# Kernel tuning notes

Measured on AMD Instinct MI355X. Metric: run time of the kernel, lower is better.

The kernel has to match this reference:

```python
import jax, jax.numpy as jnp
import numpy as np

NTYPES = 2
NATOMS = (512, 512)
N = 1024          # total atoms
NN = 128          # neighbors per type
M = NTYPES * NN   # 256 neighbor slots per atom
D = 25            # last embedding width
FH = 240          # fitting hidden width
B = 8
RMIN, RMAX = 5.8, 6.0


def _embed_mlp(s, W0, b0, W1, b1, W2, b2):
    # DeepMD-style resnet embedding net: 1 -> D -> D -> D, tanh + skip
    h = jnp.tanh(s @ W0 + b0)
    h = h + jnp.tanh(h @ W1 + b1)
    h = h + jnp.tanh(h @ W2 + b2)
    return h


def setup_inputs() -> dict:
    key = jax.random.key(0)
    ks = jax.random.split(key, 20)
    # relative positions; components in [-4.5, 4.5] so |r| spans <5.8, [5.8,6.0), >=6.0
    image_dR = (jax.random.uniform(ks[0], (B, N, NTYPES, NN, 3), jnp.float32) - 0.5) * 9.0
    # 0 == empty neighbor slot (mask = list_neigh > 0); index-1 in [0, N)
    list_neigh = jax.random.randint(ks[1], (B, N, NTYPES, NN), 0, 1025)
    davg = 0.1 * jax.random.normal(ks[2], (NTYPES, M, 4), jnp.float32)
    dstd = jax.random.uniform(ks[3], (NTYPES, M, 4), jnp.float32, 0.5, 1.5)
    P = NTYPES * NTYPES
    eW0 = jax.random.normal(ks[4], (P, 1, D), jnp.float32)
    eb0 = 0.1 * jax.random.normal(ks[5], (P, D), jnp.float32)
    eW1 = jax.random.normal(ks[6], (P, D, D), jnp.float32) / np.sqrt(D)
    eb1 = 0.1 * jax.random.normal(ks[7], (P, D), jnp.float32)
    eW2 = jax.random.normal(ks[8], (P, D, D), jnp.float32) / np.sqrt(D)
    eb2 = 0.1 * jax.random.normal(ks[9], (P, D), jnp.float32)
    fW0 = jax.random.normal(ks[10], (NTYPES, 16 * D, FH), jnp.float32) / np.sqrt(16 * D)
    fb0 = 0.1 * jax.random.normal(ks[11], (NTYPES, FH), jnp.float32)
    fW1 = jax.random.normal(ks[12], (NTYPES, FH, FH), jnp.float32) / np.sqrt(FH)
    fb1 = 0.1 * jax.random.normal(ks[13], (NTYPES, FH), jnp.float32)
    fW2 = jax.random.normal(ks[14], (NTYPES, FH, FH), jnp.float32) / np.sqrt(FH)
    fb2 = 0.1 * jax.random.normal(ks[15], (NTYPES, FH), jnp.float32)
    fW3 = jax.random.normal(ks[16], (NTYPES, FH, 1), jnp.float32) / np.sqrt(FH)
    fb3 = 0.1 * jax.random.normal(ks[17], (NTYPES, 1), jnp.float32)
    ener_shift = 0.01 * jax.random.normal(ks[18], (NTYPES,), jnp.float32)
    return {
        'image_dR': image_dR, 'list_neigh': list_neigh,
        'davg': davg, 'dstd': dstd,
        'eW0': eW0, 'eb0': eb0, 'eW1': eW1, 'eb1': eb1, 'eW2': eW2, 'eb2': eb2,
        'fW0': fW0, 'fb0': fb0, 'fW1': fW1, 'fb1': fb1, 'fW2': fW2, 'fb2': fb2,
        'fW3': fW3, 'fb3': fb3, 'ener_shift': ener_shift,
        'dfeat': jnp.zeros((1,), jnp.float32),
        'Egroup_weight': jnp.zeros((1,), jnp.float32),
        'divider': jnp.ones((1,), jnp.float32),
    }


def _forward(image_dR, list_neigh, davg, dstd,
             eW0, eb0, eW1, eb1, eW2, eb2,
             fW0, fb0, fW1, fb1, fW2, fb2, fW3, fb3, ener_shift):
    dR = image_dR.reshape(B, N, M, 3)
    neigh = list_neigh.reshape(B, N, M)
    mask = neigh > 0
    mf = mask.astype(dR.dtype)
    dR2 = jnp.sum(dR * dR, axis=-1)                       # [B,N,M]
    safe_dR2 = jnp.where(mask, dR2, 1.0)
    Rij = jnp.sqrt(safe_dR2)
    inr = mf / Rij                                        # 1/|r|, 0 off-mask
    x = Rij * mf                                          # nr = dR2/Rij = |r|
    Ri_xyz = dR / safe_dR2[..., None] * mf[..., None]     # r / |r|^2
    inr2 = inr * inr
    inr4 = inr2 * inr2
    inr3 = inr4 * x
    # smooth switching function on [RMIN, RMAX]
    u = (x - RMIN) / (RMAX - RMIN)
    poly = u * u * u * (-6.0 * u * u + 15.0 * u - 10.0) + 1.0
    dpoly = (3.0 * u * u * (-6.0 * u * u + 15.0 * u - 10.0)
             + u * u * u * (-12.0 * u + 15.0)) / (RMAX - RMIN)
    mid = (x >= RMIN) & (x < RMAX)
    vv = jnp.where(x < RMIN, 1.0, jnp.where(mid, poly, 0.0)) * mf
    dvv = jnp.where(mid, dpoly, 0.0) * mf
    Ri_pre = jnp.concatenate([inr[..., None], Ri_xyz], axis=-1)   # [B,N,M,4]
    common = (dvv * inr)[..., None] * dR                          # [B,N,M,3]
    row0 = dR * (inr3 * vv)[..., None] - Ri_pre[..., 0:1] * common
    eye = jnp.eye(3, dtype=dR.dtype)
    outer = (2.0 * dR[..., :, None] * dR[..., None, :] * inr4[..., None, None]
             - eye * inr2[..., None, None])                       # [B,N,M,3,3]
    rows = outer * vv[..., None, None] - Ri_pre[..., 1:4, None] * common[..., None, :]
    Ri_d = jnp.concatenate([row0[..., None, :], rows], axis=-2) * mf[..., None, None]  # [B,N,M,4,3]
    Ri = Ri_pre * vv[..., None]
    # per-type normalization stats broadcast over atoms of each type
    davg_res = jnp.concatenate([jnp.broadcast_to(davg[t], (NATOMS[t], M, 4)) for t in range(NTYPES)], axis=0)
    dstd_res = jnp.concatenate([jnp.broadcast_to(dstd[t], (NATOMS[t], M, 4)) for t in range(NTYPES)], axis=0)
    Ri = (Ri - davg_res) / dstd_res
    Ri_d = Ri_d / dstd_res[..., None]

    def ei_fn(Ri_n):
        Ei_list = []
        start = 0
        for t in range(NTYPES):
            na = NATOMS[t]
            Rt = jax.lax.slice_in_dim(Ri_n, start, start + na, axis=1)  # [B,na,M,4]
            acc = jnp.zeros((B, na, 4, D), Ri_n.dtype)
            for t1 in range(NTYPES):
                p = t * NTYPES + t1
                blk = Rt[:, :, t1 * NN:(t1 + 1) * NN]                  # [B,na,NN,4]
                G = _embed_mlp(blk[..., 0:1], eW0[p], eb0[p], eW1[p], eb1[p], eW2[p], eb2[p])
                acc = acc + jnp.einsum('bnkd,bnke->bnde', blk, G)
            acc = acc * (4.0 / (NN * NTYPES * 4))
            DRt = jnp.einsum('bnde,bndf->bnef', acc, acc[..., :16]).reshape(B, na, D * 16)
            h = jnp.tanh(DRt @ fW0[t] + fb0[t])
            h = h + jnp.tanh(h @ fW1[t] + fb1[t])
            h = h + jnp.tanh(h @ fW2[t] + fb2[t])
            Ei_list.append(h @ fW3[t] + fb3[t] + ener_shift[t])
            start += na
        return jnp.concatenate(Ei_list, axis=1)   # [B,N,1]

    Ei, vjpf = jax.vjp(ei_fn, Ri)
    dE, = vjpf(jnp.ones_like(Ei))                 # dEi/dRi  [B,N,M,4]
    Etot = jnp.sum(Ei, axis=1)                    # [B,1]
    pair = jnp.einsum('bnmd,bnmdx->bnmx', dE, Ri_d)   # per-pair force term [B,N,M,3]
    F_self = -jnp.sum(pair, axis=2)
    j = neigh - 1
    valid = j >= 0
    flat_idx = jnp.where(valid, j, N) + jnp.arange(B)[:, None, None] * (N + 1)
    contrib = jnp.where(valid[..., None], pair, 0.0)
    seg = jax.ops.segment_sum(contrib.reshape(-1, 3), flat_idx.reshape(-1), num_segments=B * (N + 1))
    F = F_self + seg.reshape(B, N + 1, 3)[:, :N]
    return Etot, Ei, F


def reference(image_dR, list_neigh, davg, dstd,
              eW0, eb0, eW1, eb1, eW2, eb2,
              fW0, fb0, fW1, fb1, fW2, fb2, fW3, fb3, ener_shift,
              dfeat, Egroup_weight, divider):
    # dfeat / Egroup_weight / divider are in the torch forward signature but unused
    return _forward(image_dR, list_neigh, davg, dstd,
                    eW0, eb0, eW1, eb1, eW2, eb2,
                    fW0, fb0, fW1, fb1, fW2, fb2, fW3, fb3, ener_shift)
```

## Files before the change

### kernel.cpp

```cpp
#include <hip/hip_runtime.h>

#define DEV __device__ __forceinline__

namespace {

constexpr int B_ = 8;
constexpr int N_ = 1024;
constexpr int M_ = 256;
constexpr int D_ = 25;
constexpr int FH_ = 240;
constexpr int NATOM = B_ * N_;
constexpr float CSC = 1.0f / 256.0f;

DEV float fast_tanh(float x) {
  float ax = fabsf(x);
  float e = __expf(-2.0f * ax);
  float r = (1.0f - e) * __builtin_amdgcn_rcpf(1.0f + e);
  return copysignf(r, x);
}

struct Geom {
  float mf, inr, inr2, inr4, inr3, vv, dvv;
};

DEV Geom geom_core(float dx, float dy, float dz, int nb) {
  Geom g;
  g.mf = (nb > 0) ? 1.0f : 0.0f;
  float dr2 = dx * dx + dy * dy + dz * dz;
  float safe = (nb > 0) ? dr2 : 1.0f;
  float rs = __builtin_amdgcn_rsqf(safe);
  float rij = safe * rs;
  g.inr = g.mf * rs;
  float x = rij * g.mf;
  g.inr2 = g.inr * g.inr;
  g.inr4 = g.inr2 * g.inr2;
  g.inr3 = g.inr4 * x;
  float u = (x - 5.8f) * 5.0f;
  float uu = u * u;
  float A = -6.0f * uu + 15.0f * u - 10.0f;
  float poly = uu * u * A + 1.0f;
  float dpoly = (3.0f * uu * A + uu * u * (-12.0f * u + 15.0f)) * 5.0f;
  bool mid = (x >= 5.8f) && (x < 6.0f);
  g.vv = ((x < 5.8f) ? 1.0f : (mid ? poly : 0.0f)) * g.mf;
  g.dvv = (mid ? dpoly : 0.0f) * g.mf;
  return g;
}

DEV void geom_blk(const Geom& g, float dx, float dy, float dz, int t, int m,
                  const float* __restrict__ davg, const float* __restrict__ dstd,
                  float* __restrict__ blk, float* __restrict__ rsv) {
  int bidx = (t * M_ + m) * 4;
  float4 av = *(const float4*)(davg + bidx);
  float4 sv = *(const float4*)(dstd + bidx);
  float pre[4] = {g.inr, dx * g.inr2, dy * g.inr2, dz * g.inr2};
  float avf[4] = {av.x, av.y, av.z, av.w};
  float svf[4] = {sv.x, sv.y, sv.z, sv.w};
#pragma unroll
  for (int d = 0; d < 4; ++d) {
    rsv[d] = __builtin_amdgcn_rcpf(svf[d]);
    blk[d] = (pre[d] * g.vv - avf[d]) * rsv[d];
  }
}

__global__ __launch_bounds__(256) void k_embed_acc(
    const float* __restrict__ dR, const int* __restrict__ neigh,
    const float* __restrict__ davg, const float* __restrict__ dstd,
    const float* __restrict__ eW0, const float* __restrict__ eb0,
    const float* __restrict__ eW1, const float* __restrict__ eb1,
    const float* __restrict__ eW2, const float* __restrict__ eb2,
    float* __restrict__ acc_ws) {
  __shared__ float sG[M_ * D_];
  __shared__ float4 sBlk[M_];
  int atom = blockIdx.x;
  int n = atom & (N_ - 1);
  int t = (n >= 512) ? 1 : 0;
  int m = threadIdx.x;
  int p = __builtin_amdgcn_readfirstlane(t * 2 + (m >> 7));
  const float* W0 = eW0 + p * D_;
  const float* b0 = eb0 + p * D_;
  const float* W1 = eW1 + p * D_ * D_;
  const float* b1 = eb1 + p * D_;
  const float* W2 = eW2 + p * D_ * D_;
  const float* b2 = eb2 + p * D_;
  int base = atom * M_ + m;
  float dx = dR[base * 3 + 0];
  float dy = dR[base * 3 + 1];
  float dz = dR[base * 3 + 2];
  int nb = neigh[base];
  Geom g = geom_core(dx, dy, dz, nb);
  float blk[4], rsv[4];
  geom_blk(g, dx, dy, dz, t, m, davg, dstd, blk, rsv);
  float s = blk[0];
  float h[D_], a[D_];
#pragma unroll
  for (int e = 0; e < D_; ++e) h[e] = fast_tanh(fmaf(s, W0[e], b0[e]));
#pragma unroll
  for (int e = 0; e < D_; ++e) a[e] = b1[e];
#pragma unroll
  for (int f = 0; f < D_; ++f) {
    float hf = h[f];
#pragma unroll
    for (int e = 0; e < D_; ++e) a[e] = fmaf(hf, W1[f * D_ + e], a[e]);
  }
#pragma unroll
  for (int e = 0; e < D_; ++e) h[e] += fast_tanh(a[e]);
#pragma unroll
  for (int e = 0; e < D_; ++e) a[e] = b2[e];
#pragma unroll
  for (int f = 0; f < D_; ++f) {
    float hf = h[f];
#pragma unroll
    for (int e = 0; e < D_; ++e) a[e] = fmaf(hf, W2[f * D_ + e], a[e]);
  }
#pragma unroll
  for (int e = 0; e < D_; ++e) sG[m * D_ + e] = h[e] + fast_tanh(a[e]);
  sBlk[m] = make_float4(blk[0], blk[1], blk[2], blk[3]);
  __syncthreads();
  if (threadIdx.x < 100) {
    int d = threadIdx.x & 3;
    int e = threadIdx.x >> 2;
    const float* sb = (const float*)sBlk;
    float s0 = 0.0f, s1 = 0.0f, s2 = 0.0f, s3 = 0.0f;
    for (int mm = 0; mm < M_; mm += 4) {
      s0 = fmaf(sb[(mm + 0) * 4 + d], sG[(mm + 0) * D_ + e], s0);
      s1 = fmaf(sb[(mm + 1) * 4 + d], sG[(mm + 1) * D_ + e], s1);
      s2 = fmaf(sb[(mm + 2) * 4 + d], sG[(mm + 2) * D_ + e], s2);
      s3 = fmaf(sb[(mm + 3) * 4 + d], sG[(mm + 3) * D_ + e], s3);
    }
    acc_ws[atom * 100 + d * D_ + e] = ((s0 + s1) + (s2 + s3)) * CSC;
  }
}

__global__ __launch_bounds__(256) void k_fit(
    const float* __restrict__ acc_ws,
    const float* __restrict__ fW0, const float* __restrict__ fb0,
    const float* __restrict__ fW1, const float* __restrict__ fb1,
    const float* __restrict__ fW2, const float* __restrict__ fb2,
    const float* __restrict__ fW3, const float* __restrict__ fb3,
    const float* __restrict__ ener_shift,
    float* __restrict__ dacc_ws, float* __restrict__ out) {
  constexpr int AB = 8;
  __shared__ float sAcc[AB][100];
  __shared__ float sX[AB][400];
  __shared__ float sH0[AB][FH_];
  __shared__ float sT1[AB][FH_];
  __shared__ float sH1[AB][FH_];
  __shared__ float sT2[AB][FH_];
  __shared__ float sEi[AB];
  int a0 = blockIdx.x * AB;
  int bb = a0 >> 10;
  int n0 = a0 & (N_ - 1);
  int t = (n0 >= 512) ? 1 : 0;
  int tid = threadIdx.x;
  for (int idx = tid; idx < AB * 100; idx += 256)
    ((float*)sAcc)[idx] = acc_ws[a0 * 100 + idx];
  if (tid < AB) sEi[tid] = 0.0f;
  __syncthreads();
  for (int idx = tid; idx < AB * 400; idx += 256) {
    int a = idx / 400; int r = idx % 400; int e = r >> 4; int f = r & 15;
    const float* A = sAcc[a];
    sX[a][r] = A[e] * A[f] + A[25 + e] * A[25 + f] + A[50 + e] * A[50 + f] +
               A[75 + e] * A[75 + f];
  }
  __syncthreads();
  const float* W0 = fW0 + t * 400 * FH_;
  const float* W1 = fW1 + t * FH_ * FH_;
  const float* W2 = fW2 + t * FH_ * FH_;
  const float* B0 = fb0 + t * FH_;
  const float* B1 = fb1 + t * FH_;
  const float* B2 = fb2 + t * FH_;
  const float* W3 = fW3 + t * FH_;
  int j = tid;
  if (j < FH_) {
    float acc8[AB];
#pragma unroll
    for (int a = 0; a < AB; ++a) acc8[a] = B0[j];
    for (int i = 0; i < 400; ++i) {
      float w = W0[i * FH_ + j];
#pragma unroll
      for (int a = 0; a < AB; ++a) acc8[a] = fmaf(sX[a][i], w, acc8[a]);
    }
#pragma unroll
    for (int a = 0; a < AB; ++a) sH0[a][j] = fast_tanh(acc8[a]);
  }
  __syncthreads();
  if (j < FH_) {
    float acc8[AB];
#pragma unroll
    for (int a = 0; a < AB; ++a) acc8[a] = B1[j];
    for (int f = 0; f < FH_; ++f) {
      float w = W1[f * FH_ + j];
#pragma unroll
      for (int a = 0; a < AB; ++a) acc8[a] = fmaf(sH0[a][f], w, acc8[a]);
    }
#pragma unroll
    for (int a = 0; a < AB; ++a) {
      float tv = fast_tanh(acc8[a]);
      sT1[a][j] = tv;
      sH1[a][j] = sH0[a][j] + tv;
    }
  }
  __syncthreads();
  if (j < FH_) {
    float acc8[AB];
#pragma unroll
    for (int a = 0; a < AB; ++a) acc8[a] = B2[j];
    for (int f = 0; f < FH_; ++f) {
      float w = W2[f * FH_ + j];
#pragma unroll
      for (int a = 0; a < AB; ++a) acc8[a] = fmaf(sH1[a][f], w, acc8[a]);
    }
    float w3 = W3[j];
#pragma unroll
    for (int a = 0; a < AB; ++a) {
      float tv = fast_tanh(acc8[a]);
      sT2[a][j] = tv;
      atomicAdd(&sEi[a], (sH1[a][j] + tv) * w3);
    }
  }
  __syncthreads();
  if (tid < AB) {
    float ei = sEi[tid] + fb3[t] + ener_shift[t];
    out[8 + a0 + tid] = ei;
    atomicAdd(&out[bb], ei);
  }
  if (j < FH_) {
    float w3 = W3[j];
#pragma unroll
    for (int a = 0; a < AB; ++a) {
      float tv = sT2[a][j];
      sT2[a][j] = w3 * (1.0f - tv * tv);
    }
  }
  __syncthreads();
  if (j < FH_) {
    float w3 = W3[j];
    float acc8[AB];
#pragma unroll
    for (int a = 0; a < AB; ++a) acc8[a] = w3;
    for (int k = 0; k < FH_; ++k) {
      float w = W2[j * FH_ + k];
#pragma unroll
      for (int a = 0; a < AB; ++a) acc8[a] = fmaf(sT2[a][k], w, acc8[a]);
    }
#pragma unroll
    for (int a = 0; a < AB; ++a) {
      float dh1 = acc8[a];
      float tv = sT1[a][j];
      sH1[a][j] = dh1;
      sT1[a][j] = dh1 * (1.0f - tv * tv);
    }
  }
  __syncthreads();
  if (j < FH_) {
    float acc8[AB];
#pragma unroll
    for (int a = 0; a < AB; ++a) acc8[a] = sH1[a][j];
    for (int k = 0; k < FH_; ++k) {
      float w = W1[j * FH_ + k];
#pragma unroll
      for (int a = 0; a < AB; ++a) acc8[a] = fmaf(sT1[a][k], w, acc8[a]);
    }
#pragma unroll
    for (int a = 0; a < AB; ++a) {
      float h0v = sH0[a][j];
      sH0[a][j] = acc8[a] * (1.0f - h0v * h0v);
    }
  }
  __syncthreads();
  for (int i = tid; i < 400; i += 256) {
    float acc8[AB];
#pragma unroll
    for (int a = 0; a < AB; ++a) acc8[a] = 0.0f;
    for (int jj = 0; jj < FH_; ++jj) {
      float w = W0[i * FH_ + jj];
#pragma unroll
      for (int a = 0; a < AB; ++a) acc8[a] = fmaf(sH0[a][jj], w, acc8[a]);
    }
#pragma unroll
    for (int a = 0; a < AB; ++a) sX[a][i] = acc8[a];
  }
  __syncthreads();
  for (int idx = tid; idx < AB * 100; idx += 256) {
    int a = idx / 100; int r = idx % 100; int d = r / 25; int e = r % 25;
    const float* A = sAcc[a];
    const float* DX = sX[a];
    float sum = 0.0f;
#pragma unroll
    for (int f = 0; f < 16; ++f) sum = fmaf(DX[e * 16 + f], A[d * 25 + f], sum);
    if (e < 16) {
#pragma unroll
      for (int e2 = 0; e2 < 25; ++e2) sum = fmaf(DX[e2 * 16 + e], A[d * 25 + e2], sum);
    }
    dacc_ws[a0 * 100 + idx] = sum;
  }
}

__global__ __launch_bounds__(256) __attribute__((amdgpu_waves_per_eu(2, 5)))
void k_bwd_force(
    const float* __restrict__ dR, const int* __restrict__ neigh,
    const float* __restrict__ davg, const float* __restrict__ dstd,
    const float* __restrict__ eW0, const float* __restrict__ eb0,
    const float* __restrict__ eW1, const float* __restrict__ eb1,
    const float* __restrict__ eW2, const float* __restrict__ eb2,
    const float* __restrict__ dacc_ws, float* __restrict__ out) {
  int atom = blockIdx.x;
  int bb = atom >> 10;
  int n = atom & (N_ - 1);
  int t = (n >= 512) ? 1 : 0;
  int m = threadIdx.x;
  int p = __builtin_amdgcn_readfirstlane(t * 2 + (m >> 7));
  const float* W0 = eW0 + p * D_;
  const float* b0 = eb0 + p * D_;
  const float* W1 = eW1 + p * D_ * D_;
  const float* b1 = eb1 + p * D_;
  const float* W2 = eW2 + p * D_ * D_;
  const float* b2 = eb2 + p * D_;
  const float* dac = dacc_ws + atom * 100;
  int base = atom * M_ + m;
  float dx = dR[base * 3 + 0];
  float dy = dR[base * 3 + 1];
  float dz = dR[base * 3 + 2];
  int nb = neigh[base];
  Geom g = geom_core(dx, dy, dz, nb);
  float blk[4], rsv[4];
  geom_blk(g, dx, dy, dz, t, m, davg, dstd, blk, rsv);

  float s = blk[0];
  float h[D_], hp[D_];
#pragma unroll
  for (int e = 0; e < D_; ++e) {
    float th = fast_tanh(fmaf(s, W0[e], b0[e]));
    h[e] = th;
    hp[e] = (1.0f - th * th) * W0[e];
  }
  {
    float a[D_], ap[D_];
#pragma unroll
    for (int e = 0; e < D_; ++e) { a[e] = b1[e]; ap[e] = 0.0f; }
#pragma unroll
    for (int f = 0; f < D_; ++f) {
      float hf = h[f], gf = hp[f];
#pragma unroll
      for (int e = 0; e < D_; ++e) {
        float w = W1[f * D_ + e];
        a[e] = fmaf(hf, w, a[e]);
        ap[e] = fmaf(gf, w, ap[e]);
      }
    }
#pragma unroll
    for (int e = 0; e < D_; ++e) {
      float th = fast_tanh(a[e]);
      h[e] += th;
      hp[e] = fmaf(1.0f - th * th, ap[e], hp[e]);
    }
  }
  {
    float a[D_], ap[D_];
#pragma unroll
    for (int e = 0; e < D_; ++e) { a[e] = b2[e]; ap[e] = 0.0f; }
#pragma unroll
    for (int f = 0; f < D_; ++f) {
      float hf = h[f], gf = hp[f];
#pragma unroll
      for (int e = 0; e < D_; ++e) {
        float w = W2[f * D_ + e];
        a[e] = fmaf(hf, w, a[e]);
        ap[e] = fmaf(gf, w, ap[e]);
      }
    }
#pragma unroll
    for (int e = 0; e < D_; ++e) {
      float th = fast_tanh(a[e]);
      h[e] += th;
      hp[e] = fmaf(1.0f - th * th, ap[e], hp[e]);
    }
  }

  float ds = 0.0f, db0 = 0.0f, db1 = 0.0f, db2 = 0.0f, db3 = 0.0f;
#pragma unroll
  for (int e = 0; e < D_; ++e) {
    float d0 = dac[e], d1 = dac[25 + e], d2 = dac[50 + e], d3 = dac[75 + e];
    float gG = d0 * blk[0] + d1 * blk[1] + d2 * blk[2] + d3 * blk[3];
    ds = fmaf(gG, hp[e], ds);
    float he = h[e];
    db0 = fmaf(d0, he, db0);
    db1 = fmaf(d1, he, db1);
    db2 = fmaf(d2, he, db2);
    db3 = fmaf(d3, he, db3);
  }
  float dE0 = (db0 + ds) * CSC;
  float dE1 = db1 * CSC, dE2 = db2 * CSC, dE3 = db3 * CSC;

  float dv[3] = {dx, dy, dz};
  float pre1[3] = {dx * g.inr2, dy * g.inr2, dz * g.inr2};
  float ci = g.dvv * g.inr;
  float com[3];
#pragma unroll
  for (int c = 0; c < 3; ++c) com[c] = ci * dv[c];
  float iv = g.inr3 * g.vv;
  float pc[3];
  float f0 = dE0 * rsv[0];
#pragma unroll
  for (int c = 0; c < 3; ++c) pc[c] = f0 * (dv[c] * iv - g.inr * com[c]);
  float dEr[3] = {dE1, dE2, dE3};
#pragma unroll
  for (int r = 0; r < 3; ++r) {
    float fr = dEr[r] * rsv[1 + r];
#pragma unroll
    for (int c = 0; c < 3; ++c) {
      float outer = 2.0f * dv[r] * dv[c] * g.inr4 - ((r == c) ? g.inr2 : 0.0f);
      pc[c] = fmaf(fr, outer * g.vv - pre1[r] * com[c], pc[c]);
    }
  }
  float px = pc[0] * g.mf, py = pc[1] * g.mf, pz = pc[2] * g.mf;

  if (nb > 0) {
    int jn = nb - 1;
    int fi = 8 + NATOM + (bb * N_ + jn) * 3;
    atomicAdd(&out[fi + 0], px);
    atomicAdd(&out[fi + 1], py);
    atomicAdd(&out[fi + 2], pz);
  }
#pragma unroll
  for (int i = 1; i < 64; i <<= 1) {
    px += __shfl_xor(px, i);
    py += __shfl_xor(py, i);
    pz += __shfl_xor(pz, i);
  }
  if ((m & 63) == 0) {
    int fi = 8 + NATOM + atom * 3;
    atomicAdd(&out[fi + 0], -px);
    atomicAdd(&out[fi + 1], -py);
    atomicAdd(&out[fi + 2], -pz);
  }
}

}

extern "C" void kernel_launch(void* const* d_in, const int* in_sizes, int n_in,
                              void* d_out, int out_size, void* d_ws, size_t ws_size,
                              hipStream_t stream) {
  (void)in_sizes; (void)n_in; (void)ws_size;
  const float* image_dR   = (const float*)d_in[0];
  const int*   list_neigh = (const int*)d_in[1];
  const float* davg       = (const float*)d_in[2];
  const float* dstd       = (const float*)d_in[3];
  const float* eW0        = (const float*)d_in[4];
  const float* eb0        = (const float*)d_in[5];
  const float* eW1        = (const float*)d_in[6];
  const float* eb1        = (const float*)d_in[7];
  const float* eW2        = (const float*)d_in[8];
  const float* eb2        = (const float*)d_in[9];
  const float* fW0        = (const float*)d_in[10];
  const float* fb0        = (const float*)d_in[11];
  const float* fW1        = (const float*)d_in[12];
  const float* fb1        = (const float*)d_in[13];
  const float* fW2        = (const float*)d_in[14];
  const float* fb2        = (const float*)d_in[15];
  const float* fW3        = (const float*)d_in[16];
  const float* fb3        = (const float*)d_in[17];
  const float* ener_shift = (const float*)d_in[18];
  float* out = (float*)d_out;
  float* acc_ws  = (float*)d_ws;
  float* dacc_ws = acc_ws + NATOM * 100;

  hipMemsetAsync(d_out, 0, (size_t)out_size * sizeof(float), stream);
  k_embed_acc<<<NATOM, 256, 0, stream>>>(image_dR, list_neigh, davg, dstd,
                                         eW0, eb0, eW1, eb1, eW2, eb2, acc_ws);
  k_fit<<<NATOM / 8, 256, 0, stream>>>(acc_ws, fW0, fb0, fW1, fb1, fW2, fb2,
                                       fW3, fb3, ener_shift, dacc_ws, out);
  k_bwd_force<<<NATOM, 256, 0, stream>>>(image_dR, list_neigh, davg, dstd,
                                         eW0, eb0, eW1, eb1, eW2, eb2,
                                         dacc_ws, out);
}
```

Before: 948.4 us.

## Interleave fitting activations for float4 LDS reads and stage embed weights in LDS

The fitting kernel's shared activation buffers change from [atom][feature] to [feature][atom] layout, so each inner-loop step reads all 8 atoms with two float4 LDS loads instead of eight scalar loads. The backward-force kernel now copies the embedding weights (padded to 28-wide rows) and the per-atom dacc vector into shared memory once per block, and reads them with vectorized LDS loads instead of per-thread global/scalar loads. Its waves-per-EU upper bound is also raised. The weight staging adds a syncthreads and some LDS traffic per block, and the larger register arrays may raise register pressure.

New measurement: 944.0 us. Within noise of the previous version (-0.5%).

```diff
diff --git a/kernel.cpp b/kernel.cpp
--- a/kernel.cpp
+++ b/kernel.cpp
@@ -11,6 +11,8 @@
 constexpr int FH_ = 240;
 constexpr int NATOM = B_ * N_;
 constexpr float CSC = 1.0f / 256.0f;
+constexpr int WROW = 28;
+constexpr int WPAIR = 4 * WROW + 2 * D_ * WROW;
 
 DEV float fast_tanh(float x) {
   float ax = fabsf(x);
@@ -59,6 +61,42 @@
   for (int d = 0; d < 4; ++d) {
     rsv[d] = __builtin_amdgcn_rcpf(svf[d]);
     blk[d] = (pre[d] * g.vv - avf[d]) * rsv[d];
+  }
+}
+
+DEV void load_wrow(const float* __restrict__ wr, float* __restrict__ wrow) {
+#pragma unroll
+  for (int k = 0; k < 7; ++k) {
+    float4 qv = ((const float4*)wr)[k];
+    wrow[4 * k + 0] = qv.x;
+    wrow[4 * k + 1] = qv.y;
+    wrow[4 * k + 2] = qv.z;
+    wrow[4 * k + 3] = qv.w;
+  }
+}
+
+DEV void stage_weights(int tid, int t,
+                       const float* __restrict__ eW0, const float* __restrict__ eb0,
+                       const float* __restrict__ eW1, const float* __restrict__ eb1,
+                       const float* __restrict__ eW2, const float* __restrict__ eb2,
+                       float* __restrict__ sW) {
+  for (int idx = tid; idx < 2 * WPAIR; idx += 256) {
+    int pl = idx / WPAIR;
+    int r = idx - pl * WPAIR;
+    int pp = t * 2 + pl;
+    float v = 0.0f;
+    if (r < 28) { if (r < 25) v = eW0[pp * 25 + r]; }
+    else if (r < 56) { int e = r - 28; if (e < 25) v = eb0[pp * 25 + e]; }
+    else if (r < 84) { int e = r - 56; if (e < 25) v = eb1[pp * 25 + e]; }
+    else if (r < 112) { int e = r - 84; if (e < 25) v = eb2[pp * 25 + e]; }
+    else if (r < 112 + D_ * WROW) {
+      int rr = r - 112; int f = rr / WROW, e = rr - f * WROW;
+      if (e < 25) v = eW1[pp * 625 + f * 25 + e];
+    } else {
+      int rr = r - (112 + D_ * WROW); int f = rr / WROW, e = rr - f * WROW;
+      if (e < 25) v = eW2[pp * 625 + f * 25 + e];
+    }
+    sW[idx] = v;
   }
 }
 
@@ -141,11 +179,11 @@
     float* __restrict__ dacc_ws, float* __restrict__ out) {
   constexpr int AB = 8;
   __shared__ float sAcc[AB][100];
-  __shared__ float sX[AB][400];
-  __shared__ float sH0[AB][FH_];
-  __shared__ float sT1[AB][FH_];
-  __shared__ float sH1[AB][FH_];
-  __shared__ float sT2[AB][FH_];
+  __shared__ __align__(16) float sX[400 * AB];
+  __shared__ __align__(16) float sH0[FH_ * AB];
+  __shared__ __align__(16) float sT1[FH_ * AB];
+  __shared__ __align__(16) float sH1[FH_ * AB];
+  __shared__ __align__(16) float sT2[FH_ * AB];
   __shared__ float sEi[AB];
   int a0 = blockIdx.x * AB;
   int bb = a0 >> 10;
@@ -159,8 +197,8 @@
   for (int idx = tid; idx < AB * 400; idx += 256) {
     int a = idx / 400; int r = idx % 400; int e = r >> 4; int f = r & 15;
     const float* A = sAcc[a];
-    sX[a][r] = A[e] * A[f] + A[25 + e] * A[25 + f] + A[50 + e] * A[50 + f] +
-               A[75 + e] * A[75 + f];
+    sX[r * AB + a] = A[e] * A[f] + A[25 + e] * A[25 + f] +
+                     A[50 + e] * A[50 + f] + A[75 + e] * A[75 + f];
   }
   __syncthreads();
   const float* W0 = fW0 + t * 400 * FH_;
@@ -177,11 +215,18 @@
     for (int a = 0; a < AB; ++a) acc8[a] = B0[j];
     for (int i = 0; i < 400; ++i) {
       float w = W0[i * FH_ + j];
-#pragma unroll
-      for (int a = 0; a < AB; ++a) acc8[a] = fmaf(sX[a][i], w, acc8[a]);
-    }
-#pragma unroll
-    for (int a = 0; a < AB; ++a) sH0[a][j] = fast_tanh(acc8[a]);
+      const float4* xr = (const float4*)(sX + i * AB);
+      float4 x0 = xr[0], x1 = xr[1];
+      acc8[0] = fmaf(x0.x, w, acc8[0]); acc8[1] = fmaf(x0.y, w, acc8[1]);
+      acc8[2] = fmaf(x0.z, w, acc8[2]); acc8[3] = fmaf(x0.w, w, acc8[3]);
+      acc8[4] = fmaf(x1.x, w, acc8[4]); acc8[5] = fmaf(x1.y, w, acc8[5]);
+      acc8[6] = fmaf(x1.z, w, acc8[6]); acc8[7] = fmaf(x1.w, w, acc8[7]);
+    }
+    float4* h0 = (float4*)(sH0 + j * AB);
+    h0[0] = make_float4(fast_tanh(acc8[0]), fast_tanh(acc8[1]),
+                        fast_tanh(acc8[2]), fast_tanh(acc8[3]));
+    h0[1] = make_float4(fast_tanh(acc8[4]), fast_tanh(acc8[5]),
+                        fast_tanh(acc8[6]), fast_tanh(acc8[7]));
   }
   __syncthreads();
   if (j < FH_) {
@@ -190,14 +235,18 @@
     for (int a = 0; a < AB; ++a) acc8[a] = B1[j];
     for (int f = 0; f < FH_; ++f) {
       float w = W1[f * FH_ + j];
-#pragma unroll
-      for (int a = 0; a < AB; ++a) acc8[a] = fmaf(sH0[a][f], w, acc8[a]);
+      const float4* hr = (const float4*)(sH0 + f * AB);
+      float4 h0a = hr[0], h0b = hr[1];
+      acc8[0] = fmaf(h0a.x, w, acc8[0]); acc8[1] = fmaf(h0a.y, w, acc8[1]);
+      acc8[2] = fmaf(h0a.z, w, acc8[2]); acc8[3] = fmaf(h0a.w, w, acc8[3]);
+      acc8[4] = fmaf(h0b.x, w, acc8[4]); acc8[5] = fmaf(h0b.y, w, acc8[5]);
+      acc8[6] = fmaf(h0b.z, w, acc8[6]); acc8[7] = fmaf(h0b.w, w, acc8[7]);
     }
 #pragma unroll
     for (int a = 0; a < AB; ++a) {
       float tv = fast_tanh(acc8[a]);
-      sT1[a][j] = tv;
-      sH1[a][j] = sH0[a][j] + tv;
+      sT1[j * AB + a] = tv;
+      sH1[j * AB + a] = sH0[j * AB + a] + tv;
     }
   }
   __syncthreads();
@@ -207,15 +256,19 @@
     for (int a = 0; a < AB; ++a) acc8[a] = B2[j];
     for (int f = 0; f < FH_; ++f) {
       float w = W2[f * FH_ + j];
-#pragma unroll
-      for (int a = 0; a < AB; ++a) acc8[a] = fmaf(sH1[a][f], w, acc8[a]);
+      const float4* hr = (const float4*)(sH1 + f * AB);
+      float4 h1a = hr[0], h1b = hr[1];
+      acc8[0] = fmaf(h1a.x, w, acc8[0]); acc8[1] = fmaf(h1a.y, w, acc8[1]);
+      acc8[2] = fmaf(h1a.z, w, acc8[2]); acc8[3] = fmaf(h1a.w, w, acc8[3]);
+      acc8[4] = fmaf(h1b.x, w, acc8[4]); acc8[5] = fmaf(h1b.y, w, acc8[5]);
+      acc8[6] = fmaf(h1b.z, w, acc8[6]); acc8[7] = fmaf(h1b.w, w, acc8[7]);
     }
     float w3 = W3[j];
 #pragma unroll
     for (int a = 0; a < AB; ++a) {
       float tv = fast_tanh(acc8[a]);
-      sT2[a][j] = tv;
-      atomicAdd(&sEi[a], (sH1[a][j] + tv) * w3);
+      sT2[j * AB + a] = tv;
+      atomicAdd(&sEi[a], (sH1[j * AB + a] + tv) * w3);
     }
   }
   __syncthreads();
@@ -228,8 +281,8 @@
     float w3 = W3[j];
 #pragma unroll
     for (int a = 0; a < AB; ++a) {
-      float tv = sT2[a][j];
-      sT2[a][j] = w3 * (1.0f - tv * tv);
+      float tv = sT2[j * AB + a];
+      sT2[j * AB + a] = w3 * (1.0f - tv * tv);
     }
   }
   __syncthreads();
@@ -240,31 +293,39 @@
     for (int a = 0; a < AB; ++a) acc8[a] = w3;
     for (int k = 0; k < FH_; ++k) {
       float w = W2[j * FH_ + k];
-#pragma unroll
-      for (int a = 0; a < AB; ++a) acc8[a] = fmaf(sT2[a][k], w, acc8[a]);
+      const float4* gr = (const float4*)(sT2 + k * AB);
+      float4 g2a = gr[0], g2b = gr[1];
+      acc8[0] = fmaf(g2a.x, w, acc8[0]); acc8[1] = fmaf(g2a.y, w, acc8[1]);
+      acc8[2] = fmaf(g2a.z, w, acc8[2]); acc8[3] = fmaf(g2a.w, w, acc8[3]);
+      acc8[4] = fmaf(g2b.x, w, acc8[4]); acc8[5] = fmaf(g2b.y, w, acc8[5]);
+      acc8[6] = fmaf(g2b.z, w, acc8[6]); acc8[7] = fmaf(g2b.w, w, acc8[7]);
     }
 #pragma unroll
     for (int a = 0; a < AB; ++a) {
       float dh1 = acc8[a];
-      float tv = sT1[a][j];
-      sH1[a][j] = dh1;
-      sT1[a][j] = dh1 * (1.0f - tv * tv);
+      float tv = sT1[j * AB + a];
+      sH1[j * AB + a] = dh1;
+      sT1[j * AB + a] = dh1 * (1.0f - tv * tv);
     }
   }
   __syncthreads();
   if (j < FH_) {
     float acc8[AB];
 #pragma unroll
-    for (int a = 0; a < AB; ++a) acc8[a] = sH1[a][j];
+    for (int a = 0; a < AB; ++a) acc8[a] = sH1[j * AB + a];
     for (int k = 0; k < FH_; ++k) {
       float w = W1[j * FH_ + k];
-#pragma unroll
-      for (int a = 0; a < AB; ++a) acc8[a] = fmaf(sT1[a][k], w, acc8[a]);
+      const float4* gr = (const float4*)(sT1 + k * AB);
+      float4 g1a = gr[0], g1b = gr[1];
+      acc8[0] = fmaf(g1a.x, w, acc8[0]); acc8[1] = fmaf(g1a.y, w, acc8[1]);
+      acc8[2] = fmaf(g1a.z, w, acc8[2]); acc8[3] = fmaf(g1a.w, w, acc8[3]);
+      acc8[4] = fmaf(g1b.x, w, acc8[4]); acc8[5] = fmaf(g1b.y, w, acc8[5]);
+      acc8[6] = fmaf(g1b.z, w, acc8[6]); acc8[7] = fmaf(g1b.w, w, acc8[7]);
     }
 #pragma unroll
     for (int a = 0; a < AB; ++a) {
-      float h0v = sH0[a][j];
-      sH0[a][j] = acc8[a] * (1.0f - h0v * h0v);
+      float h0v = sH0[j * AB + a];
+      sH0[j * AB + a] = acc8[a] * (1.0f - h0v * h0v);
     }
   }
   __syncthreads();
@@ -274,29 +335,35 @@
     for (int a = 0; a < AB; ++a) acc8[a] = 0.0f;
     for (int jj = 0; jj < FH_; ++jj) {
       float w = W0[i * FH_ + jj];
-#pragma unroll
-      for (int a = 0; a < AB; ++a) acc8[a] = fmaf(sH0[a][jj], w, acc8[a]);
-    }
-#pragma unroll
-    for (int a = 0; a < AB; ++a) sX[a][i] = acc8[a];
+      const float4* gr = (const float4*)(sH0 + jj * AB);
+      float4 g0a = gr[0], g0b = gr[1];
+      acc8[0] = fmaf(g0a.x, w, acc8[0]); acc8[1] = fmaf(g0a.y, w, acc8[1]);
+      acc8[2] = fmaf(g0a.z, w, acc8[2]); acc8[3] = fmaf(g0a.w, w, acc8[3]);
+      acc8[4] = fmaf(g0b.x, w, acc8[4]); acc8[5] = fmaf(g0b.y, w, acc8[5]);
+      acc8[6] = fmaf(g0b.z, w, acc8[6]); acc8[7] = fmaf(g0b.w, w, acc8[7]);
+    }
+    float4* xw = (float4*)(sX + i * AB);
+    xw[0] = make_float4(acc8[0], acc8[1], acc8[2], acc8[3]);
+    xw[1] = make_float4(acc8[4], acc8[5], acc8[6], acc8[7]);
   }
   __syncthreads();
   for (int idx = tid; idx < AB * 100; idx += 256) {
     int a = idx / 100; int r = idx % 100; int d = r / 25; int e = r % 25;
     const float* A = sAcc[a];
-    const float* DX = sX[a];
     float sum = 0.0f;
 #pragma unroll
-    for (int f = 0; f < 16; ++f) sum = fmaf(DX[e * 16 + f], A[d * 25 + f], sum);
+    for (int f = 0; f < 16; ++f)
+      sum = fmaf(sX[(e * 16 + f) * AB + a], A[d * 25 + f], sum);
     if (e < 16) {
 #pragma unroll
-      for (int e2 = 0; e2 < 25; ++e2) sum = fmaf(DX[e2 * 16 + e], A[d * 25 + e2], sum);
+      for (int e2 = 0; e2 < 25; ++e2)
+        sum = fmaf(sX[(e2 * 16 + e) * AB + a], A[d * 25 + e2], sum);
     }
     dacc_ws[a0 * 100 + idx] = sum;
   }
 }
 
-__global__ __launch_bounds__(256) __attribute__((amdgpu_waves_per_eu(2, 5)))
+__global__ __launch_bounds__(256) __attribute__((amdgpu_waves_per_eu(2, 8)))
 void k_bwd_force(
     const float* __restrict__ dR, const int* __restrict__ neigh,
     const float* __restrict__ davg, const float* __restrict__ dstd,
@@ -304,19 +371,17 @@
     const float* __restrict__ eW1, const float* __restrict__ eb1,
     const float* __restrict__ eW2, const float* __restrict__ eb2,
     const float* __restrict__ dacc_ws, float* __restrict__ out) {
+  __shared__ __align__(16) float sW[2 * WPAIR];
+  __shared__ float sDac[100];
   int atom = blockIdx.x;
   int bb = atom >> 10;
   int n = atom & (N_ - 1);
   int t = (n >= 512) ? 1 : 0;
   int m = threadIdx.x;
-  int p = __builtin_amdgcn_readfirstlane(t * 2 + (m >> 7));
-  const float* W0 = eW0 + p * D_;
-  const float* b0 = eb0 + p * D_;
-  const float* W1 = eW1 + p * D_ * D_;
-  const float* b1 = eb1 + p * D_;
-  const float* W2 = eW2 + p * D_ * D_;
-  const float* b2 = eb2 + p * D_;
-  const float* dac = dacc_ws + atom * 100;
+  stage_weights(m, t, eW0, eb0, eW1, eb1, eW2, eb2, sW);
+  for (int idx = m; idx < 100; idx += 256) sDac[idx] = dacc_ws[atom * 100 + idx];
+  __syncthreads();
+  const float* wp = sW + (m >> 7) * WPAIR;
   int base = atom * M_ + m;
   float dx = dR[base * 3 + 0];
   float dy = dR[base * 3 + 1];
@@ -328,24 +393,34 @@
 
   float s = blk[0];
   float h[D_], hp[D_];
-#pragma unroll
-  for (int e = 0; e < D_; ++e) {
-    float th = fast_tanh(fmaf(s, W0[e], b0[e]));
-    h[e] = th;
-    hp[e] = (1.0f - th * th) * W0[e];
+  {
+    float w0r[WROW], b0r[WROW];
+    load_wrow(wp, w0r);
+    load_wrow(wp + WROW, b0r);
+#pragma unroll
+    for (int e = 0; e < D_; ++e) {
+      float th = fast_tanh(fmaf(s, w0r[e], b0r[e]));
+      h[e] = th;
+      hp[e] = (1.0f - th * th) * w0r[e];
+    }
   }
   {
     float a[D_], ap[D_];
-#pragma unroll
-    for (int e = 0; e < D_; ++e) { a[e] = b1[e]; ap[e] = 0.0f; }
+    {
+      float b1r[WROW];
+      load_wrow(wp + 2 * WROW, b1r);
+#pragma unroll
+      for (int e = 0; e < D_; ++e) { a[e] = b1r[e]; ap[e] = 0.0f; }
+    }
 #pragma unroll
     for (int f = 0; f < D_; ++f) {
+      float wrow[WROW];
+      load_wrow(wp + 4 * WROW + f * WROW, wrow);
       float hf = h[f], gf = hp[f];
 #pragma unroll
       for (int e = 0; e < D_; ++e) {
-        float w = W1[f * D_ + e];
-        a[e] = fmaf(hf, w, a[e]);
-        ap[e] = fmaf(gf, w, ap[e]);
+        a[e] = fmaf(hf, wrow[e], a[e]);
+        ap[e] = fmaf(gf, wrow[e], ap[e]);
       }
     }
 #pragma unroll
@@ -357,16 +432,21 @@
   }
   {
     float a[D_], ap[D_];
-#pragma unroll
-    for (int e = 0; e < D_; ++e) { a[e] = b2[e]; ap[e] = 0.0f; }
+    {
+      float b2r[WROW];
+      load_wrow(wp + 3 * WROW, b2r);
+#pragma unroll
+      for (int e = 0; e < D_; ++e) { a[e] = b2r[e]; ap[e] = 0.0f; }
+    }
 #pragma unroll
     for (int f = 0; f < D_; ++f) {
+      float wrow[WROW];
+      load_wrow(wp + (4 + D_) * WROW + f * WROW, wrow);
       float hf = h[f], gf = hp[f];
 #pragma unroll
       for (int e = 0; e < D_; ++e) {
-        float w = W2[f * D_ + e];
-        a[e] = fmaf(hf, w, a[e]);
-        ap[e] = fmaf(gf, w, ap[e]);
+        a[e] = fmaf(hf, wrow[e], a[e]);
+        ap[e] = fmaf(gf, wrow[e], ap[e]);
       }
     }
 #pragma unroll
@@ -380,7 +460,7 @@
   float ds = 0.0f, db0 = 0.0f, db1 = 0.0f, db2 = 0.0f, db3 = 0.0f;
 #pragma unroll
   for (int e = 0; e < D_; ++e) {
-    float d0 = dac[e], d1 = dac[25 + e], d2 = dac[50 + e], d3 = dac[75 + e];
+    float d0 = sDac[e], d1 = sDac[25 + e], d2 = sDac[50 + e], d3 = sDac[75 + e];
     float gG = d0 * blk[0] + d1 * blk[1] + d2 * blk[2] + d3 * blk[3];
     ds = fmaf(gG, hp[e], ds);
     float he = h[e];
```
